# Performance work log

Measured on AMD Instinct MI355X. Metric: run time of the kernel, lower is better.

The kernel has to match this reference:

```python
import jax, jax.numpy as jnp
import numpy as np

N_DIM = 256
N_HEAD = 8
HEAD_DIM = N_DIM // N_HEAD  # 32


def setup_inputs() -> dict:
    key = jax.random.key(0)
    k_x, k_wqkv, k_bqkv, k_wp, k_bp = jax.random.split(key, 5)
    B, T, C = 32, 512, N_DIM
    x = jax.random.normal(k_x, (B, T, C), dtype=jnp.float32)
    # nn.Linear default init ~ U(-1/sqrt(fan_in), 1/sqrt(fan_in)); use scaled normal for simplicity
    s = 1.0 / np.sqrt(C)
    W_qkv = jax.random.normal(k_wqkv, (C, 3 * C), dtype=jnp.float32) * s
    b_qkv = jax.random.normal(k_bqkv, (3 * C,), dtype=jnp.float32) * s
    W_proj = jax.random.normal(k_wp, (C, C), dtype=jnp.float32) * s
    b_proj = jax.random.normal(k_bp, (C,), dtype=jnp.float32) * s
    return {"x": x, "W_qkv": W_qkv, "b_qkv": b_qkv, "W_proj": W_proj, "b_proj": b_proj}


def reference(x, W_qkv, b_qkv, W_proj, b_proj):
    B, T, C = x.shape
    H, D = N_HEAD, HEAD_DIM
    qkv = jnp.einsum('btc,cf->btf', x, W_qkv) + b_qkv  # [B,T,3C]
    q, k, v = jnp.split(qkv, 3, axis=2)
    # [B,T,C] -> [B,H,T,D]
    q = q.reshape(B, T, H, D).transpose(0, 2, 1, 3)
    k = k.reshape(B, T, H, D).transpose(0, 2, 1, 3)
    v = v.reshape(B, T, H, D).transpose(0, 2, 1, 3)
    scale = 1.0 / jnp.sqrt(jnp.float32(D))
    scores = jnp.einsum('bhqd,bhkd->bhqk', q, k) * scale  # [B,H,T,T]
    causal = jnp.tril(jnp.ones((T, T), dtype=bool))
    scores = jnp.where(causal, scores, jnp.finfo(scores.dtype).min)
    attn = jax.nn.softmax(scores, axis=-1)
    out = jnp.einsum('bhqk,bhkd->bhqd', attn, v)  # [B,H,T,D]
    out = out.transpose(0, 2, 1, 3).reshape(B, T, C)
    return jnp.einsum('btc,cf->btf', out, W_proj) + b_proj
```

## Files before the change

### kernel.cpp

```cpp
#include <hip/hip_runtime.h>
#include <stdint.h>
#include <stddef.h>

#define NB 32
#define NT 512
#define NC 256
#define NH 8
#define ND 32
#define NQTOT (NB*NH*NT*ND)

typedef __attribute__((ext_vector_type(8))) short short8;
typedef __attribute__((ext_vector_type(4))) float f32x4;

__device__ __forceinline__ unsigned short f2bf(float f) {
    union { float f; unsigned u; } x; x.f = f;
    unsigned r = (x.u + 0x7FFFu + ((x.u >> 16) & 1u)) >> 16;
    return (unsigned short)r;
}

__global__ __launch_bounds__(256) void k_cvt_wT(const float* __restrict__ w,
                                                unsigned short* __restrict__ wt, int K, int N) {
    __shared__ float tile[32][33];
    const int tx = threadIdx.x & 31;
    const int ty = threadIdx.x >> 5;
    const int n0 = blockIdx.x * 32;
    const int k0 = blockIdx.y * 32;
#pragma unroll
    for (int dy = 0; dy < 4; ++dy) {
        const int k = ty + dy * 8;
        tile[k][tx] = w[(size_t)(k0 + k) * N + n0 + tx];
    }
    __syncthreads();
#pragma unroll
    for (int dy = 0; dy < 4; ++dy) {
        const int n = ty + dy * 8;
        wt[(size_t)(n0 + n) * K + k0 + tx] = f2bf(tile[tx][n]);
    }
}

template <int EPI>
__global__ __launch_bounds__(256) void k_gemm(const void* __restrict__ Av,
                                              const unsigned short* __restrict__ Bt,
                                              const float* __restrict__ bias,
                                              unsigned short* __restrict__ qkv,
                                              float* __restrict__ outf,
                                              int M, int N, int K) {
    __shared__ unsigned short Al[2][128][40];
    __shared__ unsigned short Bl[2][128][40];

    const int tid = threadIdx.x;
    const int lane = tid & 63;
    const int w = tid >> 6;
    const int wm = w >> 1, wn = w & 1;
    const int i16 = lane & 15, g = lane >> 4;

    const int nbm = M >> 7;
    const int bm = blockIdx.x % nbm;
    const int bn = blockIdx.x / nbm;
    const int m0 = bm << 7, n0 = bn << 7;

    const float* Af = (const float*)Av;
    const unsigned short* Ab = (const unsigned short*)Av;

    f32x4 acc[4][4];
    const f32x4 z4 = {0.f, 0.f, 0.f, 0.f};
#pragma unroll
    for (int a = 0; a < 4; a++)
#pragma unroll
        for (int b = 0; b < 4; b++) acc[a][b] = z4;

    const int row0 = tid >> 2;
    const int cr = tid & 3;

    float4 fa[2][2];
    short8 sa[2];
    short8 sb[2];

    auto LOAD = [&](int k0) {
#pragma unroll
        for (int h = 0; h < 2; ++h) {
            const int row = row0 + h * 64;
            if (EPI == 0) {
                const float* p = &Af[(size_t)(m0 + row) * K + k0 + cr * 8];
                fa[h][0] = *reinterpret_cast<const float4*>(p);
                fa[h][1] = *reinterpret_cast<const float4*>(p + 4);
            } else {
                sa[h] = *reinterpret_cast<const short8*>(&Ab[(size_t)(m0 + row) * K + k0 + cr * 8]);
            }
            sb[h] = *reinterpret_cast<const short8*>(&Bt[(size_t)(n0 + row) * K + k0 + cr * 8]);
        }
    };
    auto STORE = [&](int buf) {
#pragma unroll
        for (int h = 0; h < 2; ++h) {
            const int row = row0 + h * 64;
            if (EPI == 0) {
                short8 t;
                t[0] = (short)f2bf(fa[h][0].x); t[1] = (short)f2bf(fa[h][0].y);
                t[2] = (short)f2bf(fa[h][0].z); t[3] = (short)f2bf(fa[h][0].w);
                t[4] = (short)f2bf(fa[h][1].x); t[5] = (short)f2bf(fa[h][1].y);
                t[6] = (short)f2bf(fa[h][1].z); t[7] = (short)f2bf(fa[h][1].w);
                *reinterpret_cast<short8*>(&Al[buf][row][cr * 8]) = t;
            } else {
                *reinterpret_cast<short8*>(&Al[buf][row][cr * 8]) = sa[h];
            }
            *reinterpret_cast<short8*>(&Bl[buf][row][cr * 8]) = sb[h];
        }
    };

    LOAD(0);
    STORE(0);
    __syncthreads();

    const int nk = K >> 5;
    for (int it = 0; it < nk; ++it) {
        const int cur = it & 1;
        if (it + 1 < nk) LOAD((it + 1) << 5);

        short8 af[4], bf[4];
#pragma unroll
        for (int mi = 0; mi < 4; mi++)
            af[mi] = *reinterpret_cast<const short8*>(&Al[cur][wm * 64 + mi * 16 + i16][g * 8]);
#pragma unroll
        for (int ni = 0; ni < 4; ni++)
            bf[ni] = *reinterpret_cast<const short8*>(&Bl[cur][wn * 64 + ni * 16 + i16][g * 8]);
#pragma unroll
        for (int mi = 0; mi < 4; mi++)
#pragma unroll
            for (int ni = 0; ni < 4; ni++)
                acc[mi][ni] = __builtin_amdgcn_mfma_f32_16x16x32_bf16(af[mi], bf[ni], acc[mi][ni], 0, 0, 0);

        if (it + 1 < nk) STORE(cur ^ 1);
        __syncthreads();
    }

#pragma unroll
    for (int mi = 0; mi < 4; mi++) {
#pragma unroll
        for (int ni = 0; ni < 4; ni++) {
            const int col = n0 + wn * 64 + ni * 16 + i16;
            const float bv = bias[col];
#pragma unroll
            for (int r = 0; r < 4; r++) {
                const int rowg = m0 + wm * 64 + mi * 16 + g * 4 + r;
                const float v = acc[mi][ni][r] + bv;
                if (EPI == 0) {
                    const int which = col >> 8;
                    const int cc = col & 255;
                    const int h = cc >> 5, d = cc & 31;
                    const int bb = rowg >> 9, t = rowg & 511;
                    qkv[(size_t)which * NQTOT +
                        ((((size_t)bb * NH + h) * NT + t) * ND) + d] = f2bf(v);
                } else {
                    outf[(size_t)rowg * N + col] = v;
                }
            }
        }
    }
}

__global__ __launch_bounds__(256) void k_attn(const unsigned short* __restrict__ qkv,
                                              unsigned short* __restrict__ Ob) {
    __shared__ unsigned short Vt[2][32][64];
    __shared__ unsigned short Pl[4][16][72];

    const int tid = threadIdx.x;
    const int lane = tid & 63;
    const int w = tid >> 6;
    const int i16 = lane & 15, g = lane >> 4;

    const int qc = blockIdx.x & 7;
    const int bh = blockIdx.x >> 3;
    const unsigned short* Qp = qkv + (size_t)bh * NT * ND;
    const unsigned short* Kp = qkv + (size_t)NQTOT + (size_t)bh * NT * ND;
    const unsigned short* Vp = qkv + (size_t)2 * NQTOT + (size_t)bh * NT * ND;
    const int qwave = qc * 64 + w * 16;
    const int q = qwave + i16;

    const short8 qf = *reinterpret_cast<const short8*>(&Qp[q * ND + g * 8]);

    const f32x4 z4 = {0.f, 0.f, 0.f, 0.f};
    f32x4 O0 = z4, O1 = z4;
    float m_ = -3e38f, l_ = 0.f;

    const int srow = tid >> 2;
    const int scr = tid & 3;
    const float scale2 = 0.17677669529663687f * 1.4426950408889634f;

    {
        short8 v = *reinterpret_cast<const short8*>(&Vp[srow * ND + scr * 8]);
#pragma unroll
        for (int j = 0; j < 8; j++) {
            const int swz = j ^ (scr << 1);
            Vt[0][scr * 8 + j][(srow & 7) + 8 * ((srow >> 3) ^ swz)] = (unsigned short)v[j];
        }
    }
    short8 kr[4];
#pragma unroll
    for (int kc = 0; kc < 4; kc++)
        kr[kc] = *reinterpret_cast<const short8*>(&Kp[(kc * 16 + i16) * ND + g * 8]);
    __syncthreads();

    for (int kt = 0; kt <= qc; ++kt) {
        const int cur = kt & 1;
        const bool haveNext = (kt < qc);

        short8 vnx, kn[4];
        if (haveNext) {
            vnx = *reinterpret_cast<const short8*>(&Vp[((kt + 1) * 64 + srow) * ND + scr * 8]);
#pragma unroll
            for (int kc = 0; kc < 4; kc++)
                kn[kc] = *reinterpret_cast<const short8*>(
                    &Kp[((kt + 1) * 64 + kc * 16 + i16) * ND + g * 8]);
        }

        short8 vf[2][2];
#pragma unroll
        for (int kc2 = 0; kc2 < 2; kc2++)
#pragma unroll
            for (int dh = 0; dh < 2; dh++) {
                const int dd = dh * 16 + i16;
                const int swzd = (dd & 7) ^ (((dd >> 3) & 3) << 1);
                vf[kc2][dh] = *reinterpret_cast<const short8*>(
                    &Vt[cur][dd][8 * ((kc2 * 4 + g) ^ swzd)]);
            }

        const bool diag = (kt == qc);
        float s[4][4];
#pragma unroll
        for (int kc = 0; kc < 4; kc++) {
            if (!diag || kc <= w) {
                f32x4 sv = __builtin_amdgcn_mfma_f32_16x16x32_bf16(kr[kc], qf, z4, 0, 0, 0);
                if (diag && kc == w) {
#pragma unroll
                    for (int r = 0; r < 4; r++)
                        s[kc][r] = (g * 4 + r <= i16) ? sv[r] * scale2 : -3e38f;
                } else {
#pragma unroll
                    for (int r = 0; r < 4; r++) s[kc][r] = sv[r] * scale2;
                }
            } else {
#pragma unroll
                for (int r = 0; r < 4; r++) s[kc][r] = -3e38f;
            }
        }

        float tm = fmaxf(fmaxf(fmaxf(s[0][0], s[0][1]), fmaxf(s[0][2], s[0][3])),
                         fmaxf(fmaxf(s[1][0], s[1][1]), fmaxf(s[1][2], s[1][3])));
        tm = fmaxf(tm, fmaxf(fmaxf(fmaxf(s[2][0], s[2][1]), fmaxf(s[2][2], s[2][3])),
                             fmaxf(fmaxf(s[3][0], s[3][1]), fmaxf(s[3][2], s[3][3]))));
        tm = fmaxf(tm, __shfl_xor(tm, 16, 64));
        tm = fmaxf(tm, __shfl_xor(tm, 32, 64));
        const float nm = fmaxf(m_, tm);
        const float fr = exp2f(m_ - nm);
        m_ = nm;
        float ps = 0.f;
#pragma unroll
        for (int kc = 0; kc < 4; kc++)
#pragma unroll
            for (int r = 0; r < 4; r++) {
                s[kc][r] = exp2f(s[kc][r] - nm);
                ps += s[kc][r];
            }
        ps += __shfl_xor(ps, 16, 64);
        ps += __shfl_xor(ps, 32, 64);
        l_ = l_ * fr + ps;
        O0 *= fr; O1 *= fr;

#pragma unroll
        for (int kc = 0; kc < 4; kc++) {
            ushort4 pk;
            pk.x = f2bf(s[kc][0]); pk.y = f2bf(s[kc][1]);
            pk.z = f2bf(s[kc][2]); pk.w = f2bf(s[kc][3]);
            *reinterpret_cast<ushort4*>(&Pl[w][i16][kc * 16 + g * 4]) = pk;
        }
        asm volatile("s_waitcnt lgkmcnt(0)" ::: "memory");
        __builtin_amdgcn_sched_barrier(0);

#pragma unroll
        for (int kc2 = 0; kc2 < 2; kc2++) {
            short8 pf = *reinterpret_cast<const short8*>(&Pl[w][i16][kc2 * 32 + g * 8]);
            O0 = __builtin_amdgcn_mfma_f32_16x16x32_bf16(vf[kc2][0], pf, O0, 0, 0, 0);
            O1 = __builtin_amdgcn_mfma_f32_16x16x32_bf16(vf[kc2][1], pf, O1, 0, 0, 0);
        }

        if (haveNext) {
#pragma unroll
            for (int j = 0; j < 8; j++) {
                const int swz = j ^ (scr << 1);
                Vt[cur ^ 1][scr * 8 + j][(srow & 7) + 8 * ((srow >> 3) ^ swz)] = (unsigned short)vnx[j];
            }
#pragma unroll
            for (int kc = 0; kc < 4; kc++) kr[kc] = kn[kc];
        }
        __syncthreads();
    }

    const int b = bh >> 3, h = bh & 7;
    const float inv = 1.f / l_;
    const size_t base = ((size_t)(b * NT + q)) * NC + h * 32;
    ushort4 o0, o1;
    o0.x = f2bf(O0[0] * inv); o0.y = f2bf(O0[1] * inv);
    o0.z = f2bf(O0[2] * inv); o0.w = f2bf(O0[3] * inv);
    o1.x = f2bf(O1[0] * inv); o1.y = f2bf(O1[1] * inv);
    o1.z = f2bf(O1[2] * inv); o1.w = f2bf(O1[3] * inv);
    *reinterpret_cast<ushort4*>(&Ob[base + g * 4]) = o0;
    *reinterpret_cast<ushort4*>(&Ob[base + 16 + g * 4]) = o1;
}

extern "C" void kernel_launch(void* const* d_in, const int* in_sizes, int n_in,
                              void* d_out, int out_size, void* d_ws, size_t ws_size,
                              hipStream_t stream) {
    const float* x     = (const float*)d_in[0];
    const float* Wqkv  = (const float*)d_in[1];
    const float* bqkv  = (const float*)d_in[2];
    const float* Wproj = (const float*)d_in[3];
    const float* bproj = (const float*)d_in[4];
    float* out = (float*)d_out;

    unsigned short* WqkvT  = (unsigned short*)d_ws;
    unsigned short* WprojT = WqkvT + (size_t)768 * 256;
    unsigned short* QKV    = WprojT + (size_t)256 * 256;
    unsigned short* Ob     = QKV + (size_t)3 * NQTOT;

    k_cvt_wT<<<dim3(24, 8), 256, 0, stream>>>(Wqkv, WqkvT, 256, 768);
    k_cvt_wT<<<dim3(8, 8), 256, 0, stream>>>(Wproj, WprojT, 256, 256);

    k_gemm<0><<<128 * 6, 256, 0, stream>>>(x, WqkvT, bqkv, QKV, nullptr, 16384, 768, 256);
    k_attn<<<2048, 256, 0, stream>>>(QKV, Ob);
    k_gemm<1><<<128 * 2, 256, 0, stream>>>(Ob, WprojT, bproj, nullptr, out, 16384, 256, 256);
}
```

Measured before the change: 142.4 us.

## Restructure attention so each wave owns 64 queries and V is staged once

The attention kernel now launches 512 blocks, each covering half of one (batch, head). The block's V rows are transposed into LDS once up front, and each wave processes four 16-query subtiles against K fragments read straight from global memory, with no per-tile block barriers. This is meant to reuse each K fragment across four query subtiles and drop the double-buffered synchronisation, at the cost of far fewer waves, a larger LDS footprint and uneven causal work across waves. Separately, the two weight-conversion kernels are merged into one launch to save launch overhead.

```diff
diff --git a/kernel.cpp b/kernel.cpp
--- a/kernel.cpp
+++ b/kernel.cpp
@@ -18,24 +18,26 @@
     return (unsigned short)r;
 }
 
-__global__ __launch_bounds__(256) void k_cvt_wT(const float* __restrict__ w,
-                                                unsigned short* __restrict__ wt, int K, int N) {
+__global__ __launch_bounds__(256) void k_cvt_w2(const float* __restrict__ wqkv,
+                                                unsigned short* __restrict__ wqkvT,
+                                                const float* __restrict__ wproj,
+                                                unsigned short* __restrict__ wprojT) {
     __shared__ float tile[32][33];
+    int bid = blockIdx.x;
+    const float* w; unsigned short* wt; int N, bx, by;
+    if (bid < 192) { w = wqkv; wt = wqkvT; N = 768; bx = bid % 24; by = bid / 24; }
+    else { bid -= 192; w = wproj; wt = wprojT; N = 256; bx = bid % 8; by = bid / 8; }
+    const int K = 256;
     const int tx = threadIdx.x & 31;
     const int ty = threadIdx.x >> 5;
-    const int n0 = blockIdx.x * 32;
-    const int k0 = blockIdx.y * 32;
-#pragma unroll
-    for (int dy = 0; dy < 4; ++dy) {
-        const int k = ty + dy * 8;
-        tile[k][tx] = w[(size_t)(k0 + k) * N + n0 + tx];
-    }
+    const int n0 = bx * 32, k0 = by * 32;
+#pragma unroll
+    for (int dy = 0; dy < 4; ++dy)
+        tile[ty + dy * 8][tx] = w[(size_t)(k0 + ty + dy * 8) * N + n0 + tx];
     __syncthreads();
 #pragma unroll
-    for (int dy = 0; dy < 4; ++dy) {
-        const int n = ty + dy * 8;
-        wt[(size_t)(n0 + n) * K + k0 + tx] = f2bf(tile[tx][n]);
-    }
+    for (int dy = 0; dy < 4; ++dy)
+        wt[(size_t)(n0 + ty + dy * 8) * K + k0 + tx] = f2bf(tile[tx][ty + dy * 8]);
 }
 
 template <int EPI>
@@ -161,7 +163,7 @@
 
 __global__ __launch_bounds__(256) void k_attn(const unsigned short* __restrict__ qkv,
                                               unsigned short* __restrict__ Ob) {
-    __shared__ unsigned short Vt[2][32][64];
+    __shared__ unsigned short Vt[32][512];
     __shared__ unsigned short Pl[4][16][72];
 
     const int tid = threadIdx.x;
@@ -169,51 +171,50 @@
     const int w = tid >> 6;
     const int i16 = lane & 15, g = lane >> 4;
 
-    const int qc = blockIdx.x & 7;
-    const int bh = blockIdx.x >> 3;
+    const int half = blockIdx.x >> 8;
+    const int bh = blockIdx.x & 255;
     const unsigned short* Qp = qkv + (size_t)bh * NT * ND;
     const unsigned short* Kp = qkv + (size_t)NQTOT + (size_t)bh * NT * ND;
     const unsigned short* Vp = qkv + (size_t)2 * NQTOT + (size_t)bh * NT * ND;
-    const int qwave = qc * 64 + w * 16;
-    const int q = qwave + i16;
-
-    const short8 qf = *reinterpret_cast<const short8*>(&Qp[q * ND + g * 8]);
-
-    const f32x4 z4 = {0.f, 0.f, 0.f, 0.f};
-    f32x4 O0 = z4, O1 = z4;
-    float m_ = -3e38f, l_ = 0.f;
+
+    const int qbase = half * 256 + w * 64;
+    const int ktmax = half * 4 + w;
+    const int npass = (half + 1) * 4;
 
     const int srow = tid >> 2;
     const int scr = tid & 3;
-    const float scale2 = 0.17677669529663687f * 1.4426950408889634f;
-
-    {
-        short8 v = *reinterpret_cast<const short8*>(&Vp[srow * ND + scr * 8]);
+
+    for (int p = 0; p < npass; ++p) {
+        short8 v = *reinterpret_cast<const short8*>(&Vp[(p * 64 + srow) * ND + scr * 8]);
 #pragma unroll
         for (int j = 0; j < 8; j++) {
             const int swz = j ^ (scr << 1);
-            Vt[0][scr * 8 + j][(srow & 7) + 8 * ((srow >> 3) ^ swz)] = (unsigned short)v[j];
-        }
-    }
-    short8 kr[4];
-#pragma unroll
-    for (int kc = 0; kc < 4; kc++)
-        kr[kc] = *reinterpret_cast<const short8*>(&Kp[(kc * 16 + i16) * ND + g * 8]);
+            Vt[scr * 8 + j][p * 64 + (srow & 7) + 8 * ((srow >> 3) ^ swz)] = (unsigned short)v[j];
+        }
+    }
+
+    short8 qf[4];
+#pragma unroll
+    for (int s = 0; s < 4; s++)
+        qf[s] = *reinterpret_cast<const short8*>(&Qp[(qbase + s * 16 + i16) * ND + g * 8]);
+
+    const f32x4 z4 = {0.f, 0.f, 0.f, 0.f};
+    f32x4 O[4][2];
+    float m_[4], l_[4];
+#pragma unroll
+    for (int s = 0; s < 4; s++) {
+        O[s][0] = z4; O[s][1] = z4; m_[s] = -3e38f; l_[s] = 0.f;
+    }
+
     __syncthreads();
 
-    for (int kt = 0; kt <= qc; ++kt) {
-        const int cur = kt & 1;
-        const bool haveNext = (kt < qc);
-
-        short8 vnx, kn[4];
-        if (haveNext) {
-            vnx = *reinterpret_cast<const short8*>(&Vp[((kt + 1) * 64 + srow) * ND + scr * 8]);
-#pragma unroll
-            for (int kc = 0; kc < 4; kc++)
-                kn[kc] = *reinterpret_cast<const short8*>(
-                    &Kp[((kt + 1) * 64 + kc * 16 + i16) * ND + g * 8]);
-        }
-
+    const float scale2 = 0.17677669529663687f * 1.4426950408889634f;
+
+    for (int kt = 0; kt <= ktmax; ++kt) {
+        short8 kr[4];
+#pragma unroll
+        for (int kc = 0; kc < 4; kc++)
+            kr[kc] = *reinterpret_cast<const short8*>(&Kp[(kt * 64 + kc * 16 + i16) * ND + g * 8]);
         short8 vf[2][2];
 #pragma unroll
         for (int kc2 = 0; kc2 < 2; kc2++)
@@ -222,90 +223,86 @@
                 const int dd = dh * 16 + i16;
                 const int swzd = (dd & 7) ^ (((dd >> 3) & 3) << 1);
                 vf[kc2][dh] = *reinterpret_cast<const short8*>(
-                    &Vt[cur][dd][8 * ((kc2 * 4 + g) ^ swzd)]);
-            }
-
-        const bool diag = (kt == qc);
-        float s[4][4];
-#pragma unroll
-        for (int kc = 0; kc < 4; kc++) {
-            if (!diag || kc <= w) {
-                f32x4 sv = __builtin_amdgcn_mfma_f32_16x16x32_bf16(kr[kc], qf, z4, 0, 0, 0);
-                if (diag && kc == w) {
-#pragma unroll
-                    for (int r = 0; r < 4; r++)
-                        s[kc][r] = (g * 4 + r <= i16) ? sv[r] * scale2 : -3e38f;
+                    &Vt[dd][kt * 64 + 8 * ((kc2 * 4 + g) ^ swzd)]);
+            }
+
+        const bool diag = (kt == ktmax);
+#pragma unroll
+        for (int sub = 0; sub < 4; ++sub) {
+            float s[4][4];
+#pragma unroll
+            for (int kc = 0; kc < 4; kc++) {
+                if (!diag || kc <= sub) {
+                    f32x4 sv = __builtin_amdgcn_mfma_f32_16x16x32_bf16(kr[kc], qf[sub], z4, 0, 0, 0);
+                    if (diag && kc == sub) {
+#pragma unroll
+                        for (int r = 0; r < 4; r++)
+                            s[kc][r] = (g * 4 + r <= i16) ? sv[r] * scale2 : -3e38f;
+                    } else {
+#pragma unroll
+                        for (int r = 0; r < 4; r++) s[kc][r] = sv[r] * scale2;
+                    }
                 } else {
 #pragma unroll
-                    for (int r = 0; r < 4; r++) s[kc][r] = sv[r] * scale2;
+                    for (int r = 0; r < 4; r++) s[kc][r] = -3e38f;
                 }
-            } else {
-#pragma unroll
-                for (int r = 0; r < 4; r++) s[kc][r] = -3e38f;
-            }
-        }
-
-        float tm = fmaxf(fmaxf(fmaxf(s[0][0], s[0][1]), fmaxf(s[0][2], s[0][3])),
-                         fmaxf(fmaxf(s[1][0], s[1][1]), fmaxf(s[1][2], s[1][3])));
-        tm = fmaxf(tm, fmaxf(fmaxf(fmaxf(s[2][0], s[2][1]), fmaxf(s[2][2], s[2][3])),
-                             fmaxf(fmaxf(s[3][0], s[3][1]), fmaxf(s[3][2], s[3][3]))));
-        tm = fmaxf(tm, __shfl_xor(tm, 16, 64));
-        tm = fmaxf(tm, __shfl_xor(tm, 32, 64));
-        const float nm = fmaxf(m_, tm);
-        const float fr = exp2f(m_ - nm);
-        m_ = nm;
-        float ps = 0.f;
-#pragma unroll
-        for (int kc = 0; kc < 4; kc++)
-#pragma unroll
-            for (int r = 0; r < 4; r++) {
-                s[kc][r] = exp2f(s[kc][r] - nm);
-                ps += s[kc][r];
-            }
-        ps += __shfl_xor(ps, 16, 64);
-        ps += __shfl_xor(ps, 32, 64);
-        l_ = l_ * fr + ps;
-        O0 *= fr; O1 *= fr;
-
-#pragma unroll
-        for (int kc = 0; kc < 4; kc++) {
-            ushort4 pk;
-            pk.x = f2bf(s[kc][0]); pk.y = f2bf(s[kc][1]);
-            pk.z = f2bf(s[kc][2]); pk.w = f2bf(s[kc][3]);
-            *reinterpret_cast<ushort4*>(&Pl[w][i16][kc * 16 + g * 4]) = pk;
-        }
-        asm volatile("s_waitcnt lgkmcnt(0)" ::: "memory");
-        __builtin_amdgcn_sched_barrier(0);
-
-#pragma unroll
-        for (int kc2 = 0; kc2 < 2; kc2++) {
-            short8 pf = *reinterpret_cast<const short8*>(&Pl[w][i16][kc2 * 32 + g * 8]);
-            O0 = __builtin_amdgcn_mfma_f32_16x16x32_bf16(vf[kc2][0], pf, O0, 0, 0, 0);
-            O1 = __builtin_amdgcn_mfma_f32_16x16x32_bf16(vf[kc2][1], pf, O1, 0, 0, 0);
-        }
-
-        if (haveNext) {
-#pragma unroll
-            for (int j = 0; j < 8; j++) {
-                const int swz = j ^ (scr << 1);
-                Vt[cur ^ 1][scr * 8 + j][(srow & 7) + 8 * ((srow >> 3) ^ swz)] = (unsigned short)vnx[j];
-            }
-#pragma unroll
-            for (int kc = 0; kc < 4; kc++) kr[kc] = kn[kc];
-        }
-        __syncthreads();
+            }
+
+            float tm = fmaxf(fmaxf(fmaxf(s[0][0], s[0][1]), fmaxf(s[0][2], s[0][3])),
+                             fmaxf(fmaxf(s[1][0], s[1][1]), fmaxf(s[1][2], s[1][3])));
+            tm = fmaxf(tm, fmaxf(fmaxf(fmaxf(s[2][0], s[2][1]), fmaxf(s[2][2], s[2][3])),
+                                 fmaxf(fmaxf(s[3][0], s[3][1]), fmaxf(s[3][2], s[3][3]))));
+            tm = fmaxf(tm, __shfl_xor(tm, 16, 64));
+            tm = fmaxf(tm, __shfl_xor(tm, 32, 64));
+            const float nm = fmaxf(m_[sub], tm);
+            const float fr = exp2f(m_[sub] - nm);
+            m_[sub] = nm;
+            float ps = 0.f;
+#pragma unroll
+            for (int kc = 0; kc < 4; kc++)
+#pragma unroll
+                for (int r = 0; r < 4; r++) {
+                    s[kc][r] = exp2f(s[kc][r] - nm);
+                    ps += s[kc][r];
+                }
+            ps += __shfl_xor(ps, 16, 64);
+            ps += __shfl_xor(ps, 32, 64);
+            l_[sub] = l_[sub] * fr + ps;
+            O[sub][0] *= fr; O[sub][1] *= fr;
+
+#pragma unroll
+            for (int kc = 0; kc < 4; kc++) {
+                ushort4 pk;
+                pk.x = f2bf(s[kc][0]); pk.y = f2bf(s[kc][1]);
+                pk.z = f2bf(s[kc][2]); pk.w = f2bf(s[kc][3]);
+                *reinterpret_cast<ushort4*>(&Pl[w][i16][kc * 16 + g * 4]) = pk;
+            }
+            asm volatile("s_waitcnt lgkmcnt(0)" ::: "memory");
+            __builtin_amdgcn_sched_barrier(0);
+
+#pragma unroll
+            for (int kc2 = 0; kc2 < 2; kc2++) {
+                short8 pf = *reinterpret_cast<const short8*>(&Pl[w][i16][kc2 * 32 + g * 8]);
+                O[sub][0] = __builtin_amdgcn_mfma_f32_16x16x32_bf16(vf[kc2][0], pf, O[sub][0], 0, 0, 0);
+                O[sub][1] = __builtin_amdgcn_mfma_f32_16x16x32_bf16(vf[kc2][1], pf, O[sub][1], 0, 0, 0);
+            }
+        }
     }
 
     const int b = bh >> 3, h = bh & 7;
-    const float inv = 1.f / l_;
-    const size_t base = ((size_t)(b * NT + q)) * NC + h * 32;
-    ushort4 o0, o1;
-    o0.x = f2bf(O0[0] * inv); o0.y = f2bf(O0[1] * inv);
-    o0.z = f2bf(O0[2] * inv); o0.w = f2bf(O0[3] * inv);
-    o1.x = f2bf(O1[0] * inv); o1.y = f2bf(O1[1] * inv);
-    o1.z = f2bf(O1[2] * inv); o1.w = f2bf(O1[3] * inv);
-    *reinterpret_cast<ushort4*>(&Ob[base + g * 4]) = o0;
-    *reinterpret_cast<ushort4*>(&Ob[base + 16 + g * 4]) = o1;
+#pragma unroll
+    for (int sub = 0; sub < 4; ++sub) {
+        const float inv = 1.f / l_[sub];
+        const int q = qbase + sub * 16 + i16;
+        const size_t base = ((size_t)(b * NT + q)) * NC + h * 32;
+        ushort4 o0, o1;
+        o0.x = f2bf(O[sub][0][0] * inv); o0.y = f2bf(O[sub][0][1] * inv);
+        o0.z = f2bf(O[sub][0][2] * inv); o0.w = f2bf(O[sub][0][3] * inv);
+        o1.x = f2bf(O[sub][1][0] * inv); o1.y = f2bf(O[sub][1][1] * inv);
+        o1.z = f2bf(O[sub][1][2] * inv); o1.w = f2bf(O[sub][1][3] * inv);
+        *reinterpret_cast<ushort4*>(&Ob[base + g * 4]) = o0;
+        *reinterpret_cast<ushort4*>(&Ob[base + 16 + g * 4]) = o1;
+    }
 }
 
 extern "C" void kernel_launch(void* const* d_in, const int* in_sizes, int n_in,
@@ -323,10 +320,9 @@
     unsigned short* QKV    = WprojT + (size_t)256 * 256;
     unsigned short* Ob     = QKV + (size_t)3 * NQTOT;
 
-    k_cvt_wT<<<dim3(24, 8), 256, 0, stream>>>(Wqkv, WqkvT, 256, 768);
-    k_cvt_wT<<<dim3(8, 8), 256, 0, stream>>>(Wproj, WprojT, 256, 256);
+    k_cvt_w2<<<256, 256, 0, stream>>>(Wqkv, WqkvT, Wproj, WprojT);
 
     k_gemm<0><<<128 * 6, 256, 0, stream>>>(x, WqkvT, bqkv, QKV, nullptr, 16384, 768, 256);
-    k_attn<<<2048, 256, 0, stream>>>(QKV, Ob);
+    k_attn<<<512, 256, 0, stream>>>(QKV, Ob);
     k_gemm<1><<<128 * 2, 256, 0, stream>>>(Ob, WprojT, bproj, nullptr, out, 16384, 256, 256);
 }
```

Result: faster. 129.5 us (-9.1%).
